# Kernel tuning notes

Measured on AMD Instinct MI355X. Metric: run time of the kernel, lower is better.

Reference implementation:

```python
import jax, jax.numpy as jnp
import numpy as np

B, T = 64, 20
V, E, VIS, H, L = 20000, 512, 512, 512, 49


def setup_inputs() -> dict:
    key = jax.random.key(0)
    ks = jax.random.split(key, 16)
    n = lambda k, s: jax.random.normal(k, s, dtype=jnp.float32) * 0.02
    return {
        "feature_0": jax.random.normal(ks[0], (B, 2048), jnp.float32),
        "features": jax.random.normal(ks[1], (B, 512, 1, 7, 7), jnp.float32),
        "eng_embedding": jax.random.normal(ks[2], (B, 15, 512), jnp.float32),
        "captions": jax.random.randint(ks[3], (B, T), 0, V),
        # forward assumes batch sorted by length descending
        "lengths": jnp.sort(jax.random.randint(ks[4], (B,), 1, T + 1))[::-1],
        "embed_W": n(ks[5], (V, E)),
        "W_ih": n(ks[6], (4 * H, E + VIS)),
        "W_hh": n(ks[7], (4 * H, H)),
        "b_ih": jnp.zeros((4 * H,), jnp.float32),
        "b_hh": jnp.zeros((4 * H,), jnp.float32),
        "fc_out_W": n(ks[8], (V, H)),
        "fc_out_b": jnp.zeros((V,), jnp.float32),
        "att_vw_W": n(ks[9], (VIS, VIS)),
        "att_hw_W": n(ks[10], (VIS, H)),
        "att_bias": jnp.zeros((L,), jnp.float32),
        "att_w_W": n(ks[11], (1, VIS)),
        "att_fc_v_W": n(ks[12], (VIS, VIS)),
        "att_fc_v_b": jnp.zeros((VIS,), jnp.float32),
        "img_embed_W": n(ks[13], (512, 2048)),
        "img_embed_b": jnp.zeros((512,), jnp.float32),
    }


def reference(feature_0, features, eng_embedding, captions, lengths,
              embed_W, W_ih, W_hh, b_ih, b_hh, fc_out_W, fc_out_b,
              att_vw_W, att_hw_W, att_bias, att_w_W,
              att_fc_v_W, att_fc_v_b, img_embed_W, img_embed_b):
    Bb, Tt = captions.shape
    # get_attn_input, attn_option='v': [B,512,1,7,7] -> [B,49,512], fc + L2-normalize
    f = features[:, :, 0].reshape(Bb, features.shape[1], -1).transpose(0, 2, 1)  # [B,49,512]
    fv = f @ att_fc_v_W.T + att_fc_v_b
    fv = fv / jnp.maximum(jnp.linalg.norm(fv, axis=2, keepdims=True), 1e-12)
    feas0 = feature_0 @ img_embed_W.T + img_embed_b  # [B,512], used at step 0
    we = embed_W[captions]  # [B,T,E] (dropout disabled: ratio>=1)
    # attention context for step t>0 depends only on word embedding at t-1 -> vectorize over time
    att_fea = fv @ att_vw_W.T                       # [B,L,VIS]
    att_h = we[:, :Tt - 1] @ att_hw_W.T             # [B,T-1,VIS]
    full = jax.nn.relu(att_fea[:, None] + att_h[:, :, None] + att_bias[None, None, :, None])
    att_out = full @ att_w_W[0]                     # [B,T-1,L]
    alpha = jax.nn.softmax(att_out, axis=-1)
    ctx = jnp.einsum('btl,bld->btd', alpha, fv)     # [B,T-1,VIS]
    feas_seq = jnp.concatenate([feas0[:, None], ctx], axis=1)  # [B,T,VIS]
    inputs = jnp.concatenate([feas_seq, we], axis=-1)          # [B,T,VIS+E]
    xg = jnp.einsum('bti,gi->btg', inputs, W_ih) + b_ih        # [B,T,4H]
    Hd = W_hh.shape[1]
    # length-truncated batches (sorted descending) == masked update per step
    mask_seq = jnp.arange(Tt)[:, None] < lengths[None, :]      # [T,B]

    def step(carry, xs):
        h, c = carry
        xg_t, m = xs
        g = xg_t + h @ W_hh.T + b_hh
        i, fg, gg, o = jnp.split(g, 4, axis=1)
        c_new = jax.nn.sigmoid(fg) * c + jax.nn.sigmoid(i) * jnp.tanh(gg)
        h_new = jax.nn.sigmoid(o) * jnp.tanh(c_new)
        mm = m[:, None]
        h = jnp.where(mm, h_new, h)
        c = jnp.where(mm, c_new, c)
        logits = h @ fc_out_W.T + fc_out_b
        out = jnp.where(mm, logits, jnp.zeros((), logits.dtype))
        return (h, c), out

    h0 = jnp.zeros((Bb, Hd), xg.dtype)
    _, outs = jax.lax.scan(step, (h0, h0), (xg.transpose(1, 0, 2), mask_seq))
    return outs.transpose(1, 0, 2)  # predicts [B,T,V]
```

## Files before the change

kernel.cpp:

```cpp
#include <hip/hip_runtime.h>
#include <math.h>

#define Bb 64
#define Tt 20
#define Vv 20000
#define Ee 512
#define Hh 512
#define Ll 49

typedef __attribute__((ext_vector_type(8))) short bf16x8;
typedef __attribute__((ext_vector_type(4))) float f32x4;

__device__ inline ushort f2bf(float x) {
  uint u = __builtin_bit_cast(uint, x);
  u += 0x7fffu + ((u >> 16) & 1u);
  return (ushort)(u >> 16);
}

struct Cvt8 {
  const float* s[8];
  ushort* d[8];
  int cum8[9];
};

__global__ __launch_bounds__(256) void cvt_k(Cvt8 p, int total8) {
  for (int i = blockIdx.x * 256 + threadIdx.x; i < total8;
       i += gridDim.x * 256) {
    int seg = 0;
    while (i >= p.cum8[seg + 1]) ++seg;
    const int j = i - p.cum8[seg];
    const float4* sp = (const float4*)p.s[seg];
    const float4 a = sp[j * 2];
    const float4 b = sp[j * 2 + 1];
    ushort r[8] = {f2bf(a.x), f2bf(a.y), f2bf(a.z), f2bf(a.w),
                   f2bf(b.x), f2bf(b.y), f2bf(b.z), f2bf(b.w)};
    ((uint4*)p.d[seg])[j] = *(uint4*)r;
  }
}

__global__ __launch_bounds__(256) void transpose_features_k(
    const float* __restrict__ feat, ushort* __restrict__ f2) {
  __shared__ float lds[256 * 49];
  const int b = blockIdx.x >> 1, half = blockIdx.x & 1;
  const int c0 = half * 256;
  const float* src = feat + ((size_t)b * 512 + c0) * 49;
  for (int i = threadIdx.x; i < 256 * 49; i += 256) lds[i] = src[i];
  __syncthreads();
  for (int l = 0; l < 49; ++l)
    f2[((size_t)b * 49 + l) * 512 + c0 + threadIdx.x] =
        f2bf(lds[threadIdx.x * 49 + l]);
}

template <int Kc, int MT>
__global__ __launch_bounds__(256) void gemm_mfma(
    const ushort* __restrict__ A, int lda, const ushort* __restrict__ W,
    int ldw, const float* __restrict__ bias, const float* __restrict__ addv,
    int ldadd, float* __restrict__ Cf, ushort* __restrict__ Cb, int ldc, int N,
    const int* __restrict__ lengths, int t) {
  const int wid = threadIdx.x >> 6, lane = threadIdx.x & 63;
  const int ntile = blockIdx.x * 4 + wid;
  if (ntile * 16 >= N) return;
  const int m0 = blockIdx.y * (MT * 16);
  const int ar = lane & 15;
  const int koff = (lane >> 4) * 8;
  const ushort* Ap = A + (size_t)(m0 + ar) * lda + koff;
  const ushort* Wp = W + (size_t)(ntile * 16 + ar) * ldw + koff;
  f32x4 acc[MT];
#pragma unroll
  for (int i = 0; i < MT; ++i) acc[i] = (f32x4)(0.f);
#pragma unroll 16
  for (int k0 = 0; k0 < Kc; k0 += 32) {
    const bf16x8 b = *(const bf16x8*)(Wp + k0);
#pragma unroll
    for (int mt = 0; mt < MT; ++mt) {
      const bf16x8 a = *(const bf16x8*)(Ap + (size_t)mt * 16 * lda + k0);
      acc[mt] = __builtin_amdgcn_mfma_f32_16x16x32_bf16(a, b, acc[mt], 0, 0, 0);
    }
  }
  const int col = ntile * 16 + ar;
  const float bv = bias ? bias[col] : 0.f;
#pragma unroll
  for (int mt = 0; mt < MT; ++mt) {
    const int rbase = m0 + mt * 16 + (lane >> 4) * 4;
#pragma unroll
    for (int j = 0; j < 4; ++j) {
      const int row = rbase + j;
      float v = acc[mt][j] + bv;
      if (addv) v += addv[(size_t)row * ldadd + col];
      if (lengths && t >= lengths[row]) v = 0.f;
      if (Cf) Cf[(size_t)row * ldc + col] = v;
      if (Cb) Cb[(size_t)row * ldc + col] = f2bf(v);
    }
  }
}

__global__ __launch_bounds__(256) void norm_rows_k(float* __restrict__ fv,
                                                   ushort* __restrict__ fvb,
                                                   int nrows) {
  const int row = blockIdx.x * 4 + (threadIdx.x >> 6);
  const int lane = threadIdx.x & 63;
  if (row >= nrows) return;
  float* p = fv + (size_t)row * 512;
  ushort* pb = fvb + (size_t)row * 512;
  float ss = 0.f;
  for (int d = lane; d < 512; d += 64) { float v = p[d]; ss += v * v; }
  for (int off = 32; off; off >>= 1) ss += __shfl_down(ss, off);
  ss = __shfl(ss, 0);
  const float inv = 1.f / fmaxf(sqrtf(ss), 1e-12f);
  for (int d = lane; d < 512; d += 64) {
    const float v = p[d] * inv;
    p[d] = v;
    pb[d] = f2bf(v);
  }
}

__global__ __launch_bounds__(256) void gather_embed_k(
    const int* __restrict__ captions, const float* __restrict__ embed_W,
    ushort* __restrict__ inputs) {
  const int idx = blockIdx.x * 256 + threadIdx.x;
  if (idx >= Bb * Tt * 64) return;
  const int row = idx >> 6, e8 = idx & 63;
  const int tok = captions[row];
  const float4* sp = (const float4*)(embed_W + (size_t)tok * 512 + e8 * 8);
  const float4 a = sp[0], b = sp[1];
  ushort r[8] = {f2bf(a.x), f2bf(a.y), f2bf(a.z), f2bf(a.w),
                 f2bf(b.x), f2bf(b.y), f2bf(b.z), f2bf(b.w)};
  *(uint4*)(inputs + (size_t)row * 1024 + 512 + e8 * 8) = *(uint4*)r;
}

__global__ __launch_bounds__(256) void attention_k(
    const float* __restrict__ att_fea, const float* __restrict__ att_h,
    const float* __restrict__ att_bias, const float* __restrict__ att_w,
    const float* __restrict__ fv, ushort* __restrict__ inputs) {
  const int b = blockIdx.x / 19, t = blockIdx.x % 19;
  __shared__ float hh[512];
  __shared__ float wv[512];
  __shared__ float sl[64];
  const int tid = threadIdx.x;
  const float* hp = att_h + (size_t)(b * 20 + t) * 512;
  for (int d = tid; d < 512; d += 256) { hh[d] = hp[d]; wv[d] = att_w[d]; }
  __syncthreads();
  const int wid = tid >> 6, lane = tid & 63;
  for (int l = wid; l < Ll; l += 4) {
    const float* fp = att_fea + (size_t)(b * Ll + l) * 512;
    const float bl = att_bias[l];
    float acc = 0.f;
    for (int d = lane; d < 512; d += 64) {
      float v = fp[d] + hh[d] + bl;
      acc += fmaxf(v, 0.f) * wv[d];
    }
    for (int off = 32; off; off >>= 1) acc += __shfl_down(acc, off);
    if (lane == 0) sl[l] = acc;
  }
  __syncthreads();
  if (wid == 0) {
    float v = (lane < Ll) ? sl[lane] : -INFINITY;
    float mx = v;
    for (int off = 32; off; off >>= 1) mx = fmaxf(mx, __shfl_xor(mx, off));
    float e = (lane < Ll) ? expf(v - mx) : 0.f;
    float s = e;
    for (int off = 32; off; off >>= 1) s += __shfl_xor(s, off);
    if (lane < Ll) sl[lane] = e / s;
  }
  __syncthreads();
  ushort* outp = inputs + (size_t)(b * 20 + t + 1) * 1024;
  for (int d = tid; d < 512; d += 256) {
    float acc = 0.f;
#pragma unroll 7
    for (int l = 0; l < Ll; ++l)
      acc += sl[l] * fv[(size_t)(b * Ll + l) * 512 + d];
    outp[d] = f2bf(acc);
  }
}

__global__ __launch_bounds__(256) void lstm_cell_k(
    const float* __restrict__ g, ushort* __restrict__ hb, float* __restrict__ c,
    const int* __restrict__ lengths, int t) {
  const int idx = blockIdx.x * 256 + threadIdx.x;
  if (idx >= Bb * Hh) return;
  const int b = idx >> 9, j = idx & 511;
  const float* gb = g + (size_t)b * 2048;
  const float gi = gb[j], gf = gb[512 + j], gg = gb[1024 + j],
              go = gb[1536 + j];
  const float si = 1.f / (1.f + expf(-gi));
  const float sf = 1.f / (1.f + expf(-gf));
  const float so = 1.f / (1.f + expf(-go));
  const float cn = sf * c[idx] + si * tanhf(gg);
  const float hn = so * tanhf(cn);
  if (t < lengths[b]) {
    c[idx] = cn;
    hb[idx] = f2bf(hn);
  }
}

extern "C" void kernel_launch(void* const* d_in, const int* in_sizes, int n_in,
                              void* d_out, int out_size, void* d_ws,
                              size_t ws_size, hipStream_t stream) {
  const float* feature_0 = (const float*)d_in[0];
  const float* features = (const float*)d_in[1];
  const int* captions = (const int*)d_in[3];
  const int* lengths = (const int*)d_in[4];
  const float* embed_W = (const float*)d_in[5];
  const float* W_ih = (const float*)d_in[6];
  const float* W_hh = (const float*)d_in[7];
  const float* b_ih = (const float*)d_in[8];
  const float* b_hh = (const float*)d_in[9];
  const float* fc_out_W = (const float*)d_in[10];
  const float* fc_out_b = (const float*)d_in[11];
  const float* att_vw_W = (const float*)d_in[12];
  const float* att_hw_W = (const float*)d_in[13];
  const float* att_bias = (const float*)d_in[14];
  const float* att_w_W = (const float*)d_in[15];
  const float* att_fc_v_W = (const float*)d_in[16];
  const float* att_fc_v_b = (const float*)d_in[17];
  const float* img_embed_W = (const float*)d_in[18];
  const float* img_embed_b = (const float*)d_in[19];
  float* out = (float*)d_out;

  char* ws = (char*)d_ws;
  size_t off = 0;
  auto alloc = [&](size_t bytes) {
    void* p = ws + off;
    off = (off + bytes + 255) & ~(size_t)255;
    return p;
  };
  ushort* att_fc_v_Wb = (ushort*)alloc((size_t)512 * 512 * 2);
  ushort* att_vw_Wb   = (ushort*)alloc((size_t)512 * 512 * 2);
  ushort* att_hw_Wb   = (ushort*)alloc((size_t)512 * 512 * 2);
  ushort* W_ihb       = (ushort*)alloc((size_t)2048 * 1024 * 2);
  ushort* W_hhb       = (ushort*)alloc((size_t)2048 * 512 * 2);
  ushort* fc_out_Wb   = (ushort*)alloc((size_t)Vv * 512 * 2);
  ushort* img_embedb  = (ushort*)alloc((size_t)512 * 2048 * 2);
  ushort* feature_0b  = (ushort*)alloc((size_t)Bb * 2048 * 2);
  ushort* f2      = (ushort*)alloc((size_t)Bb * Ll * 512 * 2);
  float*  fv      = (float*)alloc((size_t)Bb * Ll * 512 * 4);
  ushort* fvb     = (ushort*)alloc((size_t)Bb * Ll * 512 * 2);
  float*  att_fea = (float*)alloc((size_t)Bb * Ll * 512 * 4);
  float*  att_h   = (float*)alloc((size_t)Bb * Tt * 512 * 4);
  ushort* inputs  = (ushort*)alloc((size_t)Bb * Tt * 1024 * 2);
  float*  xg      = (float*)alloc((size_t)Bb * Tt * 2048 * 4);
  float*  g       = (float*)alloc((size_t)Bb * 2048 * 4);
  ushort* hb      = (ushort*)alloc((size_t)Bb * 512 * 2);
  float*  c       = (float*)alloc((size_t)Bb * 512 * 4);
  (void)ws_size; (void)n_in; (void)in_sizes; (void)out_size;

  Cvt8 cv;
  const float* srcs[8] = {att_fc_v_W, att_vw_W, att_hw_W, W_ih,
                          W_hh,       fc_out_W, img_embed_W, feature_0};
  ushort* dsts[8] = {att_fc_v_Wb, att_vw_Wb, att_hw_Wb, W_ihb,
                     W_hhb,       fc_out_Wb, img_embedb, feature_0b};
  const int sz8[8] = {512 * 512 / 8,   512 * 512 / 8, 512 * 512 / 8,
                      2048 * 1024 / 8, 2048 * 512 / 8, Vv * 512 / 8,
                      512 * 2048 / 8,  Bb * 2048 / 8};
  int cum = 0;
  for (int i = 0; i < 8; ++i) {
    cv.s[i] = srcs[i];
    cv.d[i] = dsts[i];
    cv.cum8[i] = cum;
    cum += sz8[i];
  }
  cv.cum8[8] = cum;
  cvt_k<<<2048, 256, 0, stream>>>(cv, cum);

  transpose_features_k<<<Bb * 2, 256, 0, stream>>>(features, f2);
  gather_embed_k<<<(Bb * Tt * 64 + 255) / 256, 256, 0, stream>>>(
      captions, embed_W, inputs);
  gemm_mfma<512, 4><<<dim3(8, 49), 256, 0, stream>>>(
      f2, 512, att_fc_v_Wb, 512, att_fc_v_b, nullptr, 0, fv, nullptr, 512, 512,
      nullptr, 0);
  norm_rows_k<<<(Bb * Ll + 3) / 4, 256, 0, stream>>>(fv, fvb, Bb * Ll);
  gemm_mfma<2048, 4><<<dim3(8, 1), 256, 0, stream>>>(
      feature_0b, 2048, img_embedb, 2048, img_embed_b, nullptr, 0, nullptr,
      inputs, Tt * 1024, 512, nullptr, 0);
  gemm_mfma<512, 4><<<dim3(8, 49), 256, 0, stream>>>(
      fvb, 512, att_vw_Wb, 512, nullptr, nullptr, 0, att_fea, nullptr, 512,
      512, nullptr, 0);
  gemm_mfma<512, 4><<<dim3(8, 20), 256, 0, stream>>>(
      inputs + 512, 1024, att_hw_Wb, 512, nullptr, nullptr, 0, att_h, nullptr,
      512, 512, nullptr, 0);
  attention_k<<<Bb * 19, 256, 0, stream>>>(att_fea, att_h, att_bias, att_w_W,
                                           fv, inputs);
  gemm_mfma<1024, 4><<<dim3(32, 20), 256, 0, stream>>>(
      inputs, 1024, W_ihb, 1024, b_ih, nullptr, 0, xg, nullptr, 2048, 2048,
      nullptr, 0);
  hipMemsetAsync(hb, 0, (size_t)Bb * 512 * 2, stream);
  hipMemsetAsync(c, 0, (size_t)Bb * 512 * 4, stream);
  for (int t = 0; t < Tt; ++t) {
    gemm_mfma<512, 1><<<dim3(32, 4), 256, 0, stream>>>(
        hb, 512, W_hhb, 512, b_hh, xg + (size_t)t * 2048, Tt * 2048, g,
        nullptr, 2048, 2048, nullptr, 0);
    lstm_cell_k<<<(Bb * Hh + 255) / 256, 256, 0, stream>>>(g, hb, c, lengths,
                                                           t);
    gemm_mfma<512, 4><<<dim3(313, 1), 256, 0, stream>>>(
        hb, 512, fc_out_Wb, 512, fc_out_b, nullptr, 0, out + (size_t)t * Vv,
        nullptr, Tt * Vv, Vv, lengths, t);
  }
}
```

Baseline: 1.036 ms.

## Fuse LSTM gate GEMM with cell update and batch output projection after recurrence

Each time step now runs one kernel that computes the h·W_hh GEMM, adds bias and the precomputed input gates, and applies the LSTM cell update through shared memory, replacing the former GEMM-plus-cell kernel pair. Hidden states are written to a sequence buffer, so the large vocabulary projection runs as one batched GEMM over all 1280 rows after the loop instead of 20 separate launches with only 64 rows each. This cuts launch count and lets the output weights be reused across more rows per tile. It costs a ping-pong pair of hidden buffers and a per-row length mask computed in the GEMM epilogue; the K loop is also restructured into 128-wide chunks.

```diff
diff --git a/kernel.cpp b/kernel.cpp
--- a/kernel.cpp
+++ b/kernel.cpp
@@ -56,7 +56,7 @@
     const ushort* __restrict__ A, int lda, const ushort* __restrict__ W,
     int ldw, const float* __restrict__ bias, const float* __restrict__ addv,
     int ldadd, float* __restrict__ Cf, ushort* __restrict__ Cb, int ldc, int N,
-    const int* __restrict__ lengths, int t) {
+    const int* __restrict__ lengths) {
   const int wid = threadIdx.x >> 6, lane = threadIdx.x & 63;
   const int ntile = blockIdx.x * 4 + wid;
   if (ntile * 16 >= N) return;
@@ -68,13 +68,17 @@
   f32x4 acc[MT];
 #pragma unroll
   for (int i = 0; i < MT; ++i) acc[i] = (f32x4)(0.f);
-#pragma unroll 16
-  for (int k0 = 0; k0 < Kc; k0 += 32) {
-    const bf16x8 b = *(const bf16x8*)(Wp + k0);
-#pragma unroll
-    for (int mt = 0; mt < MT; ++mt) {
-      const bf16x8 a = *(const bf16x8*)(Ap + (size_t)mt * 16 * lda + k0);
-      acc[mt] = __builtin_amdgcn_mfma_f32_16x16x32_bf16(a, b, acc[mt], 0, 0, 0);
+  for (int k0 = 0; k0 < Kc; k0 += 128) {
+#pragma unroll
+    for (int kk = 0; kk < 4; ++kk) {
+      const int k = k0 + kk * 32;
+      const bf16x8 b = *(const bf16x8*)(Wp + k);
+#pragma unroll
+      for (int mt = 0; mt < MT; ++mt) {
+        const bf16x8 a = *(const bf16x8*)(Ap + (size_t)mt * 16 * lda + k);
+        acc[mt] =
+            __builtin_amdgcn_mfma_f32_16x16x32_bf16(a, b, acc[mt], 0, 0, 0);
+      }
     }
   }
   const int col = ntile * 16 + ar;
@@ -87,7 +91,10 @@
       const int row = rbase + j;
       float v = acc[mt][j] + bv;
       if (addv) v += addv[(size_t)row * ldadd + col];
-      if (lengths && t >= lengths[row]) v = 0.f;
+      if (lengths) {
+        const int bidx = row / Tt, tidx = row - bidx * Tt;
+        if (tidx >= lengths[bidx]) v = 0.f;
+      }
       if (Cf) Cf[(size_t)row * ldc + col] = v;
       if (Cb) Cb[(size_t)row * ldc + col] = f2bf(v);
     }
@@ -173,23 +180,70 @@
   }
 }
 
-__global__ __launch_bounds__(256) void lstm_cell_k(
-    const float* __restrict__ g, ushort* __restrict__ hb, float* __restrict__ c,
-    const int* __restrict__ lengths, int t) {
-  const int idx = blockIdx.x * 256 + threadIdx.x;
-  if (idx >= Bb * Hh) return;
-  const int b = idx >> 9, j = idx & 511;
-  const float* gb = g + (size_t)b * 2048;
-  const float gi = gb[j], gf = gb[512 + j], gg = gb[1024 + j],
-              go = gb[1536 + j];
-  const float si = 1.f / (1.f + expf(-gi));
-  const float sf = 1.f / (1.f + expf(-gf));
-  const float so = 1.f / (1.f + expf(-go));
-  const float cn = sf * c[idx] + si * tanhf(gg);
-  const float hn = so * tanhf(cn);
-  if (t < lengths[b]) {
-    c[idx] = cn;
-    hb[idx] = f2bf(hn);
+__global__ __launch_bounds__(256) void lstm_step_k(
+    const ushort* __restrict__ hcur, ushort* __restrict__ hnext,
+    float* __restrict__ c, const ushort* __restrict__ Whh,
+    const float* __restrict__ b_hh, const float* __restrict__ xg,
+    const int* __restrict__ lengths, ushort* __restrict__ hseq, int t) {
+  __shared__ float gl[4][64][16];
+  const int wid = threadIdx.x >> 6, lane = threadIdx.x & 63;
+  const int j0 = blockIdx.x * 16;
+  const int ar = lane & 15;
+  const int koff = (lane >> 4) * 8;
+  const int n = wid * 512 + j0 + ar;
+  const ushort* Wp = Whh + (size_t)n * 512 + koff;
+  const ushort* Ap = hcur + (size_t)ar * 512 + koff;
+  f32x4 acc[4];
+#pragma unroll
+  for (int i = 0; i < 4; ++i) acc[i] = (f32x4)(0.f);
+  for (int k0 = 0; k0 < 512; k0 += 128) {
+#pragma unroll
+    for (int kk = 0; kk < 4; ++kk) {
+      const int k = k0 + kk * 32;
+      const bf16x8 b = *(const bf16x8*)(Wp + k);
+#pragma unroll
+      for (int mt = 0; mt < 4; ++mt) {
+        const bf16x8 a = *(const bf16x8*)(Ap + (size_t)mt * 16 * 512 + k);
+        acc[mt] =
+            __builtin_amdgcn_mfma_f32_16x16x32_bf16(a, b, acc[mt], 0, 0, 0);
+      }
+    }
+  }
+  const float bh = b_hh[n];
+#pragma unroll
+  for (int mt = 0; mt < 4; ++mt) {
+    const int rbase = mt * 16 + (lane >> 4) * 4;
+#pragma unroll
+    for (int j = 0; j < 4; ++j) {
+      const int row = rbase + j;
+      gl[wid][row][ar] =
+          acc[mt][j] + bh + xg[((size_t)row * Tt + t) * 2048 + n];
+    }
+  }
+  __syncthreads();
+#pragma unroll
+  for (int k = 0; k < 4; ++k) {
+    const int e = threadIdx.x + k * 256;
+    const int row = e >> 4, col = e & 15;
+    const float gi = gl[0][row][col];
+    const float gf = gl[1][row][col];
+    const float gg = gl[2][row][col];
+    const float go = gl[3][row][col];
+    const float si = 1.f / (1.f + expf(-gi));
+    const float sf = 1.f / (1.f + expf(-gf));
+    const float so = 1.f / (1.f + expf(-go));
+    const int hidx = row * 512 + j0 + col;
+    const float cn = sf * c[hidx] + si * tanhf(gg);
+    const float hn = so * tanhf(cn);
+    ushort hv;
+    if (t < lengths[row]) {
+      c[hidx] = cn;
+      hv = f2bf(hn);
+    } else {
+      hv = hcur[hidx];
+    }
+    hnext[hidx] = hv;
+    hseq[((size_t)row * Tt + t) * 512 + j0 + col] = hv;
   }
 }
 
@@ -239,8 +293,9 @@
   float*  att_h   = (float*)alloc((size_t)Bb * Tt * 512 * 4);
   ushort* inputs  = (ushort*)alloc((size_t)Bb * Tt * 1024 * 2);
   float*  xg      = (float*)alloc((size_t)Bb * Tt * 2048 * 4);
-  float*  g       = (float*)alloc((size_t)Bb * 2048 * 4);
-  ushort* hb      = (ushort*)alloc((size_t)Bb * 512 * 2);
+  ushort* hseq    = (ushort*)alloc((size_t)Bb * Tt * 512 * 2);
+  ushort* h0      = (ushort*)alloc((size_t)Bb * 512 * 2);
+  ushort* h1      = (ushort*)alloc((size_t)Bb * 512 * 2);
   float*  c       = (float*)alloc((size_t)Bb * 512 * 4);
   (void)ws_size; (void)n_in; (void)in_sizes; (void)out_size;
 
@@ -267,32 +322,34 @@
       captions, embed_W, inputs);
   gemm_mfma<512, 4><<<dim3(8, 49), 256, 0, stream>>>(
       f2, 512, att_fc_v_Wb, 512, att_fc_v_b, nullptr, 0, fv, nullptr, 512, 512,
-      nullptr, 0);
+      nullptr);
   norm_rows_k<<<(Bb * Ll + 3) / 4, 256, 0, stream>>>(fv, fvb, Bb * Ll);
   gemm_mfma<2048, 4><<<dim3(8, 1), 256, 0, stream>>>(
       feature_0b, 2048, img_embedb, 2048, img_embed_b, nullptr, 0, nullptr,
-      inputs, Tt * 1024, 512, nullptr, 0);
+      inputs, Tt * 1024, 512, nullptr);
   gemm_mfma<512, 4><<<dim3(8, 49), 256, 0, stream>>>(
       fvb, 512, att_vw_Wb, 512, nullptr, nullptr, 0, att_fea, nullptr, 512,
-      512, nullptr, 0);
+      512, nullptr);
   gemm_mfma<512, 4><<<dim3(8, 20), 256, 0, stream>>>(
       inputs + 512, 1024, att_hw_Wb, 512, nullptr, nullptr, 0, att_h, nullptr,
-      512, 512, nullptr, 0);
+      512, 512, nullptr);
   attention_k<<<Bb * 19, 256, 0, stream>>>(att_fea, att_h, att_bias, att_w_W,
                                            fv, inputs);
   gemm_mfma<1024, 4><<<dim3(32, 20), 256, 0, stream>>>(
       inputs, 1024, W_ihb, 1024, b_ih, nullptr, 0, xg, nullptr, 2048, 2048,
-      nullptr, 0);
-  hipMemsetAsync(hb, 0, (size_t)Bb * 512 * 2, stream);
+      nullptr);
+  hipMemsetAsync(h0, 0, (size_t)Bb * 512 * 2, stream);
   hipMemsetAsync(c, 0, (size_t)Bb * 512 * 4, stream);
+  const ushort* hc = h0;
+  ushort* hn = h1;
   for (int t = 0; t < Tt; ++t) {
-    gemm_mfma<512, 1><<<dim3(32, 4), 256, 0, stream>>>(
-        hb, 512, W_hhb, 512, b_hh, xg + (size_t)t * 2048, Tt * 2048, g,
-        nullptr, 2048, 2048, nullptr, 0);
-    lstm_cell_k<<<(Bb * Hh + 255) / 256, 256, 0, stream>>>(g, hb, c, lengths,
-                                                           t);
-    gemm_mfma<512, 4><<<dim3(313, 1), 256, 0, stream>>>(
-        hb, 512, fc_out_Wb, 512, fc_out_b, nullptr, 0, out + (size_t)t * Vv,
-        nullptr, Tt * Vv, Vv, lengths, t);
-  }
-}
+    lstm_step_k<<<Hh / 16, 256, 0, stream>>>(hc, hn, c, W_hhb, b_hh, xg,
+                                             lengths, hseq, t);
+    const ushort* tmp = hn;
+    hn = (ushort*)hc;
+    hc = tmp;
+  }
+  gemm_mfma<512, 8><<<dim3(313, 10), 256, 0, stream>>>(
+      hseq, 512, fc_out_Wb, 512, fc_out_b, nullptr, 0, out, nullptr, Vv, Vv,
+      lengths);
+}
```

Result: faster. 894.1 us (-13.7%).
